# Performance work log

Hardware: AMD Instinct MI355X
Metric: run time of the kernel (lower is better)

## Reference

```python
import jax, jax.numpy as jnp
import numpy as np

B, T = 4, 1024
N_EMBD, N_HEAD, N_LAYER, VOCAB = 1024, 16, 4, 32000
HEAD_DIM = N_EMBD // N_HEAD  # 64
SCALE = 0.02


def setup_inputs() -> dict:
    key = jax.random.key(0)
    ks = jax.random.split(key, 9)
    f32 = jnp.float32
    return {
        "idx": jax.random.randint(ks[0], (B, T), 0, VOCAB),
        "token_emb": jax.random.normal(ks[1], (VOCAB, N_EMBD), f32) * SCALE,
        "pos_emb": jax.random.normal(ks[2], (T, N_EMBD), f32) * SCALE,
        "wk": jax.random.normal(ks[3], (N_EMBD, N_HEAD, HEAD_DIM), f32) * SCALE,
        "wq": jax.random.normal(ks[4], (N_EMBD, N_HEAD, HEAD_DIM), f32) * SCALE,
        "wv": jax.random.normal(ks[5], (N_EMBD, N_HEAD, HEAD_DIM), f32) * SCALE,
        "w_proj": jax.random.normal(ks[6], (N_EMBD, N_HEAD, HEAD_DIM), f32) * SCALE,
        "w_in": jax.random.normal(ks[7], (N_EMBD, 4 * N_EMBD), f32) * SCALE,
        "w_out": jax.random.normal(ks[8], (4 * N_EMBD, N_EMBD), f32) * SCALE,
    }


def reference(idx, token_emb, pos_emb, wk, wq, wv, w_proj, w_in, w_out):
    # tok_emb[idx] : (B, T, C); pos_emb sliced to first T positions (no kv-cache)
    x = token_emb[idx] + pos_emb[None, :T, :]
    causal = jnp.tril(jnp.ones((T, T), dtype=bool))[None, None]  # (1,1,T,T)
    neg = jnp.asarray(-1e30, x.dtype)
    for _ in range(N_LAYER):  # weights are SHARED across layers, as in source
        # source quirk: k<-attention_k, v<-attention_q, q<-attention_v
        k = jnp.einsum("btc,cnh->bnth", x, wk)
        v = jnp.einsum("btc,cnh->bnth", x, wq)
        q = jnp.einsum("btc,cnh->bnth", x, wv)
        att = jnp.einsum("bnqh,bnkh->bnqk", q, k) * (HEAD_DIM ** -0.5)
        att = jax.nn.softmax(jnp.where(causal, att, neg), axis=-1)
        o = jnp.einsum("bnqk,bnkh->bqnh", att, v)  # (B,T,H,Hd)
        x = x + jnp.einsum("bqnh,cnh->bqc", o, w_proj)  # MHA output proj + residual
        x = x + jax.nn.relu(x @ w_in) @ w_out  # FFN + residual
    logits = x @ token_emb.T  # tied output head: (B,T,VOCAB)
    return logits
```

## Files before the change

### kernel.cpp

```cpp
#include <hip/hip_runtime.h>
#include <hip/hip_bf16.h>


using bf16 = __hip_bfloat16;
typedef __bf16 bf16x8 __attribute__((ext_vector_type(8)));
typedef float f32x4 __attribute__((ext_vector_type(4)));
typedef unsigned int u32;

#define TOK 4096
#define C 1024
#define NH 16
#define HD 64
#define TT 1024
#define FF 4096
#define VOC 32000

__device__ __forceinline__ void gl_lds16(const bf16* g, bf16* s) {
    __builtin_amdgcn_global_load_lds(
        (const __attribute__((address_space(1))) u32*)g,
        (__attribute__((address_space(3))) u32*)s, 16, 0, 0);
}

__global__ __launch_bounds__(256) void embed_kernel(
    const int* __restrict__ idx, const float* __restrict__ tok,
    const float* __restrict__ pos, float* __restrict__ xf, bf16* __restrict__ xb)
{
    int i = blockIdx.x * 256 + threadIdx.x;
    int t = i >> 10;
    int c = i & 1023;
    int ti = t & 1023;
    int v = idx[t];
    float val = tok[(size_t)v * C + c] + pos[(size_t)ti * C + c];
    xf[i] = val;
    xb[i] = (bf16)val;
}

__global__ __launch_bounds__(256) void wtrans_kernel(
    const float* __restrict__ src, bf16* __restrict__ dst, int K, int N)
{
    __shared__ float tile[64][65];
    const int bk = blockIdx.y * 64;
    const int bn = blockIdx.x * 64;
    const int tid = threadIdx.x;
    const int r = tid >> 4;
    const int c = (tid & 15) * 4;
    #pragma unroll
    for (int p = 0; p < 4; p++) {
        float4 f = *reinterpret_cast<const float4*>(src + (size_t)(bk + p * 16 + r) * N + bn + c);
        tile[p * 16 + r][c + 0] = f.x;
        tile[p * 16 + r][c + 1] = f.y;
        tile[p * 16 + r][c + 2] = f.z;
        tile[p * 16 + r][c + 3] = f.w;
    }
    __syncthreads();
    const int n = tid >> 2;
    const int k0 = (tid & 3) * 16;
    bf16 vals[16];
    #pragma unroll
    for (int j = 0; j < 16; j++) vals[j] = (bf16)tile[k0 + j][n];
    uint4* d = reinterpret_cast<uint4*>(dst + (size_t)(bn + n) * K + bk + k0);
    d[0] = reinterpret_cast<const uint4*>(vals)[0];
    d[1] = reinterpret_cast<const uint4*>(vals)[1];
}

__global__ __launch_bounds__(256) void wconv_kernel(
    const float* __restrict__ src, bf16* __restrict__ dst)
{
    size_t i = ((size_t)blockIdx.x * 256 + threadIdx.x) * 8;
    float4 a = *reinterpret_cast<const float4*>(src + i);
    float4 b = *reinterpret_cast<const float4*>(src + i + 4);
    bf16 v[8] = {(bf16)a.x, (bf16)a.y, (bf16)a.z, (bf16)a.w,
                 (bf16)b.x, (bf16)b.y, (bf16)b.z, (bf16)b.w};
    *reinterpret_cast<uint4*>(dst + i) = *reinterpret_cast<const uint4*>(v);
}

template <int EPI, int NT>
__global__ __launch_bounds__(256) void gemm128_kernel(
    const bf16* __restrict__ A, const bf16* __restrict__ Bt,
    bf16* __restrict__ Cb, float* __restrict__ Cf, float* __restrict__ Xf,
    int M, int N, int K)
{
    constexpr int BN = NT * 32;
    __shared__ __align__(16) bf16 As[128 * 64];
    __shared__ __align__(16) bf16 Bs[BN * 64];
    const int tid = threadIdx.x;
    const int lane = tid & 63;
    const int wave = tid >> 6;
    const int wr = wave >> 1;
    const int wc = wave & 1;

    const int gx = gridDim.x;
    const int nwg = gx * gridDim.y;
    int wgid = blockIdx.y * gx + blockIdx.x;
    const int cpx = nwg >> 3;
    wgid = (wgid & 7) * cpx + (wgid >> 3);
    const int bm = (wgid / gx) * 128;
    const int bn = (wgid % gx) * BN;

    f32x4 acc[4][NT] = {};

    const int srow = tid >> 3;
    const int scol = (tid & 7) * 8;

    const int m16 = lane & 15;
    const int koff = (lane >> 4) * 8;

    for (int kc = 0; kc < K; kc += 64) {
        #pragma unroll
        for (int p = 0; p < 4; p++) {
            int row = p * 32 + srow;
            gl_lds16(A + (size_t)(bm + row) * K + kc + scol, As + row * 64 + scol);
        }
        #pragma unroll
        for (int p = 0; p < BN / 32; p++) {
            int row = p * 32 + srow;
            gl_lds16(Bt + (size_t)(bn + row) * K + kc + scol, Bs + row * 64 + scol);
        }
        __syncthreads();

        #pragma unroll
        for (int ks = 0; ks < 2; ks++) {
            bf16x8 bfr[NT];
            #pragma unroll
            for (int j = 0; j < NT; j++)
                bfr[j] = *reinterpret_cast<const bf16x8*>(Bs + (wc * (NT * 16) + j * 16 + m16) * 64 + ks * 32 + koff);
            #pragma unroll
            for (int i = 0; i < 4; i++) {
                bf16x8 afr = *reinterpret_cast<const bf16x8*>(As + (wr * 64 + i * 16 + m16) * 64 + ks * 32 + koff);
                #pragma unroll
                for (int j = 0; j < NT; j++)
                    acc[i][j] = __builtin_amdgcn_mfma_f32_16x16x32_bf16(afr, bfr[j], acc[i][j], 0, 0, 0);
            }
        }
        __syncthreads();
    }

    const int r0 = (lane >> 4) * 4;
    #pragma unroll
    for (int i = 0; i < 4; i++) {
        int row = bm + wr * 64 + i * 16 + r0;
        #pragma unroll
        for (int j = 0; j < NT; j++) {
            int col = bn + wc * (NT * 16) + j * 16 + m16;
            #pragma unroll
            for (int r = 0; r < 4; r++) {
                size_t off = (size_t)(row + r) * N + col;
                float v = acc[i][j][r];
                if (EPI == 0) {
                    Cb[off] = (bf16)v;
                } else if (EPI == 1) {
                    Cb[off] = (bf16)fmaxf(v, 0.f);
                } else if (EPI == 2) {
                    float xn = Xf[off] + v;
                    Xf[off] = xn;
                    Cb[off] = (bf16)xn;
                } else {
                    Cf[off] = v;
                }
            }
        }
    }
}

__global__ __launch_bounds__(256) void vtrans_kernel(
    const bf16* __restrict__ vb, bf16* __restrict__ vt, int ld)
{
    const int kt = blockIdx.x;
    const int n  = blockIdx.y;
    const int b  = blockIdx.z;
    const int tid = threadIdx.x;
    __shared__ __align__(16) bf16 tile[64][72];
    const int r = tid >> 2;
    const int c = (tid & 3) << 4;
    {
        const uint4* src = reinterpret_cast<const uint4*>(vb + (size_t)(b * TT + kt * 64 + r) * ld + n * HD + c);
        uint4* dst = reinterpret_cast<uint4*>(&tile[r][c]);
        dst[0] = src[0];
        dst[1] = src[1];
    }
    __syncthreads();
    bf16 col[16];
    #pragma unroll
    for (int j = 0; j < 16; j++) col[j] = tile[c + j][r];
    uint4* dst = reinterpret_cast<uint4*>(vt + ((size_t)(b * NH + n) * HD + r) * TT + (size_t)kt * 64 + c);
    const uint4* srcp = reinterpret_cast<const uint4*>(col);
    dst[0] = srcp[0];
    dst[1] = srcp[1];
}

__global__ __launch_bounds__(256) void fattn_kernel(
    const bf16* __restrict__ qb, const bf16* __restrict__ kb,
    const bf16* __restrict__ vt, bf16* __restrict__ ob, int ld)
{
    const int qt  = blockIdx.x;
    const int n   = blockIdx.y;
    const int b   = blockIdx.z;
    const int tid  = threadIdx.x;
    const int lane = tid & 63;
    const int wave = tid >> 6;
    const int t0 = b * TT;

    __shared__ __align__(16) bf16 Ks[64][72];
    __shared__ __align__(16) bf16 Vs[64][72];
    __shared__ __align__(16) bf16 Ps[64][72];

    const int m16  = lane & 15;
    const int koff = (lane >> 4) * 8;
    const int qrow_in = 16 * wave + (lane >> 4) * 4;

    bf16x8 qf[2];
    {
        const bf16* qrow = qb + (size_t)(t0 + qt * 64 + 16 * wave + m16) * ld + n * HD;
        qf[0] = *reinterpret_cast<const bf16x8*>(qrow + koff);
        qf[1] = *reinterpret_cast<const bf16x8*>(qrow + 32 + koff);
    }

    f32x4 o_acc[4] = {};
    float mrow[4], lrow[4];
    #pragma unroll
    for (int r = 0; r < 4; r++) { mrow[r] = -1e30f; lrow[r] = 0.f; }

    const int r_st = tid >> 2;
    const int c_st = (tid & 3) << 4;

    for (int kt = 0; kt <= qt; kt++) {
        {
            const uint4* src = reinterpret_cast<const uint4*>(kb + (size_t)(t0 + kt * 64 + r_st) * ld + n * HD + c_st);
            uint4* dst = reinterpret_cast<uint4*>(&Ks[r_st][c_st]);
            dst[0] = src[0];
            dst[1] = src[1];
        }
        {
            const uint4* src = reinterpret_cast<const uint4*>(vt + ((size_t)(b * NH + n) * HD + r_st) * TT + (size_t)kt * 64 + c_st);
            uint4* dst = reinterpret_cast<uint4*>(&Vs[r_st][c_st]);
            dst[0] = src[0];
            dst[1] = src[1];
        }
        __syncthreads();

        f32x4 s_acc[4] = {};
        #pragma unroll
        for (int ks = 0; ks < 2; ks++) {
            #pragma unroll
            for (int nt = 0; nt < 4; nt++) {
                bf16x8 kf = *reinterpret_cast<const bf16x8*>(&Ks[16 * nt + m16][32 * ks + koff]);
                s_acc[nt] = __builtin_amdgcn_mfma_f32_16x16x32_bf16(qf[ks], kf, s_acc[nt], 0, 0, 0);
            }
        }

        #pragma unroll
        for (int nt = 0; nt < 4; nt++) {
            #pragma unroll
            for (int r = 0; r < 4; r++) s_acc[nt][r] *= 0.125f;
        }
        if (kt == qt) {
            #pragma unroll
            for (int nt = 0; nt < 4; nt++) {
                int col = m16 + 16 * nt;
                #pragma unroll
                for (int r = 0; r < 4; r++) {
                    if (col > qrow_in + r) s_acc[nt][r] = -1e30f;
                }
            }
        }

        float pmax[4];
        #pragma unroll
        for (int r = 0; r < 4; r++)
            pmax[r] = fmaxf(fmaxf(s_acc[0][r], s_acc[1][r]), fmaxf(s_acc[2][r], s_acc[3][r]));
        #pragma unroll
        for (int off = 8; off >= 1; off >>= 1) {
            #pragma unroll
            for (int r = 0; r < 4; r++) pmax[r] = fmaxf(pmax[r], __shfl_xor(pmax[r], off));
        }

        #pragma unroll
        for (int r = 0; r < 4; r++) {
            float mnew = fmaxf(mrow[r], pmax[r]);
            float corr = __expf(mrow[r] - mnew);
            mrow[r] = mnew;
            lrow[r] *= corr;
            #pragma unroll
            for (int nt = 0; nt < 4; nt++) o_acc[nt][r] *= corr;
        }

        float psum[4] = {0.f, 0.f, 0.f, 0.f};
        #pragma unroll
        for (int nt = 0; nt < 4; nt++) {
            int col = m16 + 16 * nt;
            #pragma unroll
            for (int r = 0; r < 4; r++) {
                float p = __expf(s_acc[nt][r] - mrow[r]);
                psum[r] += p;
                Ps[qrow_in + r][col] = (bf16)p;
            }
        }
        #pragma unroll
        for (int off = 8; off >= 1; off >>= 1) {
            #pragma unroll
            for (int r = 0; r < 4; r++) psum[r] += __shfl_xor(psum[r], off);
        }
        #pragma unroll
        for (int r = 0; r < 4; r++) lrow[r] += psum[r];

        __syncthreads();

        #pragma unroll
        for (int ks = 0; ks < 2; ks++) {
            bf16x8 pf = *reinterpret_cast<const bf16x8*>(&Ps[16 * wave + m16][32 * ks + koff]);
            #pragma unroll
            for (int nt = 0; nt < 4; nt++) {
                bf16x8 vf = *reinterpret_cast<const bf16x8*>(&Vs[16 * nt + m16][32 * ks + koff]);
                o_acc[nt] = __builtin_amdgcn_mfma_f32_16x16x32_bf16(pf, vf, o_acc[nt], 0, 0, 0);
            }
        }
        __syncthreads();
    }

    #pragma unroll
    for (int r = 0; r < 4; r++) {
        float invl = 1.f / lrow[r];
        int q = qt * 64 + qrow_in + r;
        #pragma unroll
        for (int nt = 0; nt < 4; nt++) {
            ob[(size_t)(t0 + q) * C + n * HD + m16 + 16 * nt] = (bf16)(o_acc[nt][r] * invl);
        }
    }
}

extern "C" void kernel_launch(void* const* d_in, const int* in_sizes, int n_in,
                              void* d_out, int out_size, void* d_ws, size_t ws_size,
                              hipStream_t stream) {
    const int*   idx    = (const int*)  d_in[0];
    const float* tok    = (const float*)d_in[1];
    const float* pos    = (const float*)d_in[2];
    const float* wk     = (const float*)d_in[3];
    const float* wq     = (const float*)d_in[4];
    const float* wv     = (const float*)d_in[5];
    const float* w_proj = (const float*)d_in[6];
    const float* w_in   = (const float*)d_in[7];
    const float* w_out  = (const float*)d_in[8];
    float* out = (float*)d_out;

    char* w = (char*)d_ws;
    float* xf     = (float*)w;   w += (size_t)TOK * C * 4;
    bf16* xb      = (bf16*)w;    w += (size_t)TOK * C * 2;
    char* alias0  = w;
    bf16* wqkvT   = (bf16*)w;    w += (size_t)3 * C * C * 2;
    bf16* wpT     = (bf16*)w;    w += (size_t)C * C * 2;
    bf16* w_inT   = (bf16*)w;    w += (size_t)C * FF * 2;
    bf16* w_outT  = (bf16*)w;    w += (size_t)C * FF * 2;
    bf16* kvq     = (bf16*)w;    w += (size_t)TOK * 3 * C * 2;
    bf16* vt      = (bf16*)w;    w += (size_t)TOK * C * 2;
    bf16* obuf    = (bf16*)w;    w += (size_t)TOK * C * 2;
    bf16* tokT = (bf16*)alias0;
    bf16* hbuf = (bf16*)d_out;

    embed_kernel<<<TOK * C / 256, 256, 0, stream>>>(idx, tok, pos, xf, xb);

    wtrans_kernel<<<dim3(C / 64, C / 64), 256, 0, stream>>>(wk, wqkvT, C, C);
    wtrans_kernel<<<dim3(C / 64, C / 64), 256, 0, stream>>>(wq, wqkvT + (size_t)C * C, C, C);
    wtrans_kernel<<<dim3(C / 64, C / 64), 256, 0, stream>>>(wv, wqkvT + (size_t)2 * C * C, C, C);
    wtrans_kernel<<<dim3(FF / 64, C / 64), 256, 0, stream>>>(w_in, w_inT, C, FF);
    wtrans_kernel<<<dim3(C / 64, FF / 64), 256, 0, stream>>>(w_out, w_outT, FF, C);
    wconv_kernel<<<C * C / 2048, 256, 0, stream>>>(w_proj, wpT);

    dim3 gQKV(3 * C / 128, TOK / 128);
    dim3 gCn(C / 64, TOK / 128);
    dim3 gF(FF / 128, TOK / 128);
    dim3 gV(VOC / 128, TOK / 128);

    for (int layer = 0; layer < 4; layer++) {
        gemm128_kernel<0, 4><<<gQKV, 256, 0, stream>>>(xb, wqkvT, kvq, nullptr, nullptr, TOK, 3 * C, C);

        vtrans_kernel<<<dim3(TT / 64, NH, 4), 256, 0, stream>>>(kvq + C, vt, 3 * C);
        fattn_kernel<<<dim3(TT / 64, NH, 4), 256, 0, stream>>>(kvq + 2 * C, kvq, vt, obuf, 3 * C);

        gemm128_kernel<2, 2><<<gCn, 256, 0, stream>>>(obuf, wpT, xb, nullptr, xf, TOK, C, C);
        gemm128_kernel<1, 4><<<gF, 256, 0, stream>>>(xb, w_inT, hbuf, nullptr, nullptr, TOK, FF, C);
        gemm128_kernel<2, 2><<<gCn, 256, 0, stream>>>(hbuf, w_outT, xb, nullptr, xf, TOK, C, FF);
    }

    wconv_kernel<<<VOC * C / 2048, 256, 0, stream>>>(tok, tokT);
    gemm128_kernel<3, 4><<<gV, 256, 0, stream>>>(xb, tokT, nullptr, out, nullptr, TOK, VOC, C);
}
```

Measured before the change: 2.140 ms.

## Widen flash-attention query tile to 128 rows and add lazy softmax rescale

The attention kernel now handles 128 query rows per block, two 16-row MFMA groups per wave. This reuses each K/V tile loaded into LDS across twice as many queries and halves the grid. It also skips the running-max rescale unless some row's max has grown by more than 8, masks probabilities explicitly, and makes the fp32 logits store nontemporal. The grid shrinks to 256 blocks with more causal imbalance per block, and register pressure rises.

```diff
diff --git a/kernel.cpp b/kernel.cpp
--- a/kernel.cpp
+++ b/kernel.cpp
@@ -155,7 +155,7 @@
                     Xf[off] = xn;
                     Cb[off] = (bf16)xn;
                 } else {
-                    Cf[off] = v;
+                    __builtin_nontemporal_store(v, &Cf[off]);
                 }
             }
         }
@@ -202,28 +202,33 @@
 
     __shared__ __align__(16) bf16 Ks[64][72];
     __shared__ __align__(16) bf16 Vs[64][72];
-    __shared__ __align__(16) bf16 Ps[64][72];
+    __shared__ __align__(16) bf16 Ps[128][72];
 
     const int m16  = lane & 15;
     const int koff = (lane >> 4) * 8;
-    const int qrow_in = 16 * wave + (lane >> 4) * 4;
-
-    bf16x8 qf[2];
-    {
-        const bf16* qrow = qb + (size_t)(t0 + qt * 64 + 16 * wave + m16) * ld + n * HD;
-        qf[0] = *reinterpret_cast<const bf16x8*>(qrow + koff);
-        qf[1] = *reinterpret_cast<const bf16x8*>(qrow + 32 + koff);
-    }
-
-    f32x4 o_acc[4] = {};
-    float mrow[4], lrow[4];
-    #pragma unroll
-    for (int r = 0; r < 4; r++) { mrow[r] = -1e30f; lrow[r] = 0.f; }
+    const int r4   = (lane >> 4) * 4;
+    const int qbase = wave * 32;
+
+    bf16x8 qf[2][2];
+    #pragma unroll
+    for (int i = 0; i < 2; i++) {
+        const bf16* qrow = qb + (size_t)(t0 + qt * 128 + qbase + i * 16 + m16) * ld + n * HD;
+        qf[i][0] = *reinterpret_cast<const bf16x8*>(qrow + koff);
+        qf[i][1] = *reinterpret_cast<const bf16x8*>(qrow + 32 + koff);
+    }
+
+    f32x4 o_acc[2][4] = {};
+    float mrow[2][4], lrow[2][4];
+    #pragma unroll
+    for (int i = 0; i < 2; i++)
+        #pragma unroll
+        for (int r = 0; r < 4; r++) { mrow[i][r] = -1e30f; lrow[i][r] = 0.f; }
 
     const int r_st = tid >> 2;
     const int c_st = (tid & 3) << 4;
 
-    for (int kt = 0; kt <= qt; kt++) {
+    const int ktmax = 2 * qt + 1;
+    for (int kt = 0; kt <= ktmax; kt++) {
         {
             const uint4* src = reinterpret_cast<const uint4*>(kb + (size_t)(t0 + kt * 64 + r_st) * ld + n * HD + c_st);
             uint4* dst = reinterpret_cast<uint4*>(&Ks[r_st][c_st]);
@@ -238,92 +243,130 @@
         }
         __syncthreads();
 
-        f32x4 s_acc[4] = {};
+        f32x4 s_acc[2][4] = {};
         #pragma unroll
         for (int ks = 0; ks < 2; ks++) {
-            #pragma unroll
-            for (int nt = 0; nt < 4; nt++) {
-                bf16x8 kf = *reinterpret_cast<const bf16x8*>(&Ks[16 * nt + m16][32 * ks + koff]);
-                s_acc[nt] = __builtin_amdgcn_mfma_f32_16x16x32_bf16(qf[ks], kf, s_acc[nt], 0, 0, 0);
+            bf16x8 kfr[4];
+            #pragma unroll
+            for (int nt = 0; nt < 4; nt++)
+                kfr[nt] = *reinterpret_cast<const bf16x8*>(&Ks[16 * nt + m16][32 * ks + koff]);
+            #pragma unroll
+            for (int i = 0; i < 2; i++)
+                #pragma unroll
+                for (int nt = 0; nt < 4; nt++)
+                    s_acc[i][nt] = __builtin_amdgcn_mfma_f32_16x16x32_bf16(qf[i][ks], kfr[nt], s_acc[i][nt], 0, 0, 0);
+        }
+
+        #pragma unroll
+        for (int i = 0; i < 2; i++)
+            #pragma unroll
+            for (int nt = 0; nt < 4; nt++)
+                #pragma unroll
+                for (int r = 0; r < 4; r++) s_acc[i][nt][r] *= 0.125f;
+        if (kt >= 2 * qt) {
+            #pragma unroll
+            for (int i = 0; i < 2; i++) {
+                int rowg = qt * 128 + qbase + i * 16 + r4;
+                #pragma unroll
+                for (int nt = 0; nt < 4; nt++) {
+                    int colg = kt * 64 + m16 + 16 * nt;
+                    #pragma unroll
+                    for (int r = 0; r < 4; r++)
+                        if (colg > rowg + r) s_acc[i][nt][r] = -1e30f;
+                }
             }
         }
 
-        #pragma unroll
-        for (int nt = 0; nt < 4; nt++) {
-            #pragma unroll
-            for (int r = 0; r < 4; r++) s_acc[nt][r] *= 0.125f;
-        }
-        if (kt == qt) {
+        float pmax[2][4];
+        #pragma unroll
+        for (int i = 0; i < 2; i++)
+            #pragma unroll
+            for (int r = 0; r < 4; r++)
+                pmax[i][r] = fmaxf(fmaxf(s_acc[i][0][r], s_acc[i][1][r]),
+                                   fmaxf(s_acc[i][2][r], s_acc[i][3][r]));
+        #pragma unroll
+        for (int off = 8; off >= 1; off >>= 1)
+            #pragma unroll
+            for (int i = 0; i < 2; i++)
+                #pragma unroll
+                for (int r = 0; r < 4; r++)
+                    pmax[i][r] = fmaxf(pmax[i][r], __shfl_xor(pmax[i][r], off));
+
+        float dm = -1e30f;
+        #pragma unroll
+        for (int i = 0; i < 2; i++)
+            #pragma unroll
+            for (int r = 0; r < 4; r++)
+                dm = fmaxf(dm, pmax[i][r] - mrow[i][r]);
+        if (__any(dm > 8.f)) {
+            #pragma unroll
+            for (int i = 0; i < 2; i++)
+                #pragma unroll
+                for (int r = 0; r < 4; r++) {
+                    float mnew = fmaxf(mrow[i][r], pmax[i][r]);
+                    float corr = __expf(mrow[i][r] - mnew);
+                    mrow[i][r] = mnew;
+                    lrow[i][r] *= corr;
+                    #pragma unroll
+                    for (int nt = 0; nt < 4; nt++) o_acc[i][nt][r] *= corr;
+                }
+        }
+
+        float psum[2][4] = {};
+        #pragma unroll
+        for (int i = 0; i < 2; i++) {
             #pragma unroll
             for (int nt = 0; nt < 4; nt++) {
                 int col = m16 + 16 * nt;
                 #pragma unroll
                 for (int r = 0; r < 4; r++) {
-                    if (col > qrow_in + r) s_acc[nt][r] = -1e30f;
+                    float sv = s_acc[i][nt][r];
+                    float p = __expf(sv - mrow[i][r]);
+                    p = (sv > -1e29f) ? p : 0.f;
+                    psum[i][r] += p;
+                    Ps[qbase + i * 16 + r4 + r][col] = (bf16)p;
                 }
             }
         }
-
-        float pmax[4];
-        #pragma unroll
-        for (int r = 0; r < 4; r++)
-            pmax[r] = fmaxf(fmaxf(s_acc[0][r], s_acc[1][r]), fmaxf(s_acc[2][r], s_acc[3][r]));
-        #pragma unroll
-        for (int off = 8; off >= 1; off >>= 1) {
-            #pragma unroll
-            for (int r = 0; r < 4; r++) pmax[r] = fmaxf(pmax[r], __shfl_xor(pmax[r], off));
-        }
-
+        #pragma unroll
+        for (int off = 8; off >= 1; off >>= 1)
+            #pragma unroll
+            for (int i = 0; i < 2; i++)
+                #pragma unroll
+                for (int r = 0; r < 4; r++) psum[i][r] += __shfl_xor(psum[i][r], off);
+        #pragma unroll
+        for (int i = 0; i < 2; i++)
+            #pragma unroll
+            for (int r = 0; r < 4; r++) lrow[i][r] += psum[i][r];
+
+        __syncthreads();
+
+        #pragma unroll
+        for (int ks = 0; ks < 2; ks++) {
+            bf16x8 vfr[4];
+            #pragma unroll
+            for (int nt = 0; nt < 4; nt++)
+                vfr[nt] = *reinterpret_cast<const bf16x8*>(&Vs[16 * nt + m16][32 * ks + koff]);
+            #pragma unroll
+            for (int i = 0; i < 2; i++) {
+                bf16x8 pf = *reinterpret_cast<const bf16x8*>(&Ps[qbase + i * 16 + m16][32 * ks + koff]);
+                #pragma unroll
+                for (int nt = 0; nt < 4; nt++)
+                    o_acc[i][nt] = __builtin_amdgcn_mfma_f32_16x16x32_bf16(pf, vfr[nt], o_acc[i][nt], 0, 0, 0);
+            }
+        }
+        __syncthreads();
+    }
+
+    #pragma unroll
+    for (int i = 0; i < 2; i++) {
         #pragma unroll
         for (int r = 0; r < 4; r++) {
-            float mnew = fmaxf(mrow[r], pmax[r]);
-            float corr = __expf(mrow[r] - mnew);
-            mrow[r] = mnew;
-            lrow[r] *= corr;
-            #pragma unroll
-            for (int nt = 0; nt < 4; nt++) o_acc[nt][r] *= corr;
-        }
-
-        float psum[4] = {0.f, 0.f, 0.f, 0.f};
-        #pragma unroll
-        for (int nt = 0; nt < 4; nt++) {
-            int col = m16 + 16 * nt;
-            #pragma unroll
-            for (int r = 0; r < 4; r++) {
-                float p = __expf(s_acc[nt][r] - mrow[r]);
-                psum[r] += p;
-                Ps[qrow_in + r][col] = (bf16)p;
-            }
-        }
-        #pragma unroll
-        for (int off = 8; off >= 1; off >>= 1) {
-            #pragma unroll
-            for (int r = 0; r < 4; r++) psum[r] += __shfl_xor(psum[r], off);
-        }
-        #pragma unroll
-        for (int r = 0; r < 4; r++) lrow[r] += psum[r];
-
-        __syncthreads();
-
-        #pragma unroll
-        for (int ks = 0; ks < 2; ks++) {
-            bf16x8 pf = *reinterpret_cast<const bf16x8*>(&Ps[16 * wave + m16][32 * ks + koff]);
-            #pragma unroll
-            for (int nt = 0; nt < 4; nt++) {
-                bf16x8 vf = *reinterpret_cast<const bf16x8*>(&Vs[16 * nt + m16][32 * ks + koff]);
-                o_acc[nt] = __builtin_amdgcn_mfma_f32_16x16x32_bf16(pf, vf, o_acc[nt], 0, 0, 0);
-            }
-        }
-        __syncthreads();
-    }
-
-    #pragma unroll
-    for (int r = 0; r < 4; r++) {
-        float invl = 1.f / lrow[r];
-        int q = qt * 64 + qrow_in + r;
-        #pragma unroll
-        for (int nt = 0; nt < 4; nt++) {
-            ob[(size_t)(t0 + q) * C + n * HD + m16 + 16 * nt] = (bf16)(o_acc[nt][r] * invl);
+            float invl = 1.f / lrow[i][r];
+            int q = qt * 128 + qbase + i * 16 + r4 + r;
+            #pragma unroll
+            for (int nt = 0; nt < 4; nt++)
+                ob[(size_t)(t0 + q) * C + n * HD + m16 + 16 * nt] = (bf16)(o_acc[i][nt][r] * invl);
         }
     }
 }
@@ -374,7 +417,7 @@
         gemm128_kernel<0, 4><<<gQKV, 256, 0, stream>>>(xb, wqkvT, kvq, nullptr, nullptr, TOK, 3 * C, C);
 
         vtrans_kernel<<<dim3(TT / 64, NH, 4), 256, 0, stream>>>(kvq + C, vt, 3 * C);
-        fattn_kernel<<<dim3(TT / 64, NH, 4), 256, 0, stream>>>(kvq + 2 * C, kvq, vt, obuf, 3 * C);
+        fattn_kernel<<<dim3(TT / 128, NH, 4), 256, 0, stream>>>(kvq + 2 * C, kvq, vt, obuf, 3 * C);
 
         gemm128_kernel<2, 2><<<gCn, 256, 0, stream>>>(obuf, wpT, xb, nullptr, xf, TOK, C, C);
         gemm128_kernel<1, 4><<<gF, 256, 0, stream>>>(xb, w_inT, hbuf, nullptr, nullptr, TOK, FF, C);
```

Measured after the change: 2.111 ms. About the same (-1.3%).
